# Kernel tuning notes

Hardware: AMD Instinct MI355X
Metric: run time of the kernel (lower is better)

Reference implementation:

```python
import jax, jax.numpy as jnp
import numpy as np

ALPHA = 0.2  # LeakyReLU negative slope
NEG_INF = -9e15


def setup_inputs() -> dict:
    key = jax.random.key(0)
    ks = jax.random.split(key, 6)
    B, N, F_in, F_out = 16, 1024, 1024, 512
    x = jax.random.normal(ks[0], (B, N, F_in), dtype=jnp.float32)
    adj = jax.random.randint(ks[1], (B, N, N), 0, 2, dtype=jnp.int32)
    W = jax.random.normal(ks[2], (F_in, F_out), dtype=jnp.float32) * 0.02
    a = jax.random.normal(ks[3], (2 * F_out, 1), dtype=jnp.float32) * 0.02
    fc_w = jax.random.normal(ks[4], (F_out, 2 * F_out), dtype=jnp.float32) * 0.02
    fc_b = jnp.zeros((F_out,), dtype=jnp.float32)
    return {"x": x, "adj": adj, "W": W, "a": a, "fc_w": fc_w, "fc_b": fc_b}


def reference(x, adj, W, a, fc_w, fc_b):
    # h: [B, N, F_out]
    h = jnp.matmul(x, W)
    F_out = W.shape[1]
    # The original builds a_input = concat(h_i, h_j) of shape [B,N,N,2F] and
    # contracts with a. Equivalently (same math, no O(N^2 F) intermediate):
    # e_ij = leakyrelu(h_i . a[:F] + h_j . a[F:])
    a1 = a[:F_out, 0]  # [F_out]
    a2 = a[F_out:, 0]  # [F_out]
    f1 = jnp.einsum('bnf,f->bn', h, a1)  # source term
    f2 = jnp.einsum('bnf,f->bn', h, a2)  # target term
    e = jax.nn.leaky_relu(f1[:, :, None] + f2[:, None, :], negative_slope=ALPHA)  # [B,N,N]
    attention = jnp.where(adj > 0, e, jnp.full_like(e, NEG_INF))
    attention = jax.nn.softmax(attention, axis=2)
    # dropout is identity in eval mode
    agg = jnp.matmul(attention, h)  # [B,N,F_out]
    h_prime = jnp.concatenate([agg, h], axis=2)  # [B,N,2F]
    h_prime = jnp.matmul(h_prime, fc_w.T) + fc_b
    return jax.nn.elu(h_prime)  # concat=True path
```

## Files before the change

kernel.cpp:

```cpp
#include <hip/hip_runtime.h>

#define ALPHA 0.2f

typedef __attribute__((ext_vector_type(8))) short short8;
typedef __attribute__((ext_vector_type(4))) float f32x4;

__device__ __forceinline__ unsigned short f2b(float f) {
  unsigned int u; __builtin_memcpy(&u, &f, 4);
  unsigned int r = (u + 0x7FFFu + ((u >> 16) & 1u)) >> 16;
  return (unsigned short)r;
}
__device__ __forceinline__ float b2f(unsigned short v) {
  unsigned int u = ((unsigned int)v) << 16; float f; __builtin_memcpy(&f, &u, 4); return f;
}
__device__ __forceinline__ void gl_lds16(const unsigned short* g, unsigned short* l) {
  __builtin_amdgcn_global_load_lds((__attribute__((address_space(1))) void*)g,
                                   (__attribute__((address_space(3))) void*)l, 16, 0, 0);
}
__device__ __forceinline__ void vm6() { asm volatile("s_waitcnt vmcnt(6)" ::: "memory"); }
__device__ __forceinline__ void vm0() { asm volatile("s_waitcnt vmcnt(0)" ::: "memory"); }
__device__ __forceinline__ void lg0() { asm volatile("s_waitcnt lgkmcnt(0)" ::: "memory"); }

__device__ __forceinline__ void cvt_f4(const float* __restrict__ in,
                                       unsigned short* __restrict__ out,
                                       unsigned int f4idx) {
  float4 v = ((const float4*)in)[f4idx];
  alignas(8) unsigned short o[4];
  o[0] = f2b(v.x); o[1] = f2b(v.y); o[2] = f2b(v.z); o[3] = f2b(v.w);
  ((uint2*)out)[f4idx] = *(const uint2*)o;
}

__global__ __launch_bounds__(256) void prep1(const float* __restrict__ x,
                                             unsigned short* __restrict__ xb,
                                             const float* __restrict__ fcw,
                                             unsigned short* __restrict__ fcwb,
                                             const float* __restrict__ W,
                                             unsigned short* __restrict__ Wt) {
  __shared__ alignas(16) unsigned short tile[64][72];
  unsigned int bx = blockIdx.x;
  unsigned int tid = threadIdx.x;
  if (bx < 8192u) {
    unsigned int base = bx * 512u;
    cvt_f4(x, xb, base + tid);
    cvt_f4(x, xb, base + 256u + tid);
  } else if (bx < 8448u) {
    unsigned int base = (bx - 8192u) * 512u;
    cvt_f4(fcw, fcwb, base + tid);
    cvt_f4(fcw, fcwb, base + 256u + tid);
  } else {
    unsigned int idx = bx - 8448u;
    unsigned int k0 = (idx >> 3) * 64, n0 = (idx & 7) * 64;
    #pragma unroll
    for (int p = 0; p < 4; p++) {
      int r = p * 16 + (tid >> 4);
      int c = (tid & 15) * 4;
      float4 v = *(const float4*)(W + (size_t)(k0 + r) * 512 + n0 + c);
      tile[r][c] = f2b(v.x); tile[r][c + 1] = f2b(v.y);
      tile[r][c + 2] = f2b(v.z); tile[r][c + 3] = f2b(v.w);
    }
    __syncthreads();
    int f = tid >> 2;
    int ic = (tid & 3) * 16;
    alignas(16) unsigned short buf[16];
    #pragma unroll
    for (int k = 0; k < 16; k++) buf[k] = tile[ic + k][f];
    uint4* dst = (uint4*)(Wt + (size_t)(n0 + f) * 1024 + k0 + ic);
    dst[0] = ((const uint4*)buf)[0];
    dst[1] = ((const uint4*)buf)[1];
  }
}

__global__ __launch_bounds__(256) void prep2(const unsigned short* __restrict__ hp,
                                             const float* __restrict__ a,
                                             float* __restrict__ f1, float* __restrict__ f2,
                                             unsigned short* __restrict__ ht) {
  __shared__ alignas(16) unsigned short tile[64][72];
  int bx = blockIdx.x;
  int tid = threadIdx.x;
  if (bx < 4096) {
    int row = bx * 4 + (tid >> 6);
    int lane = tid & 63;
    const unsigned short* hrow = hp + (size_t)row * 1024 + 512;
    uint4 raw = *(const uint4*)(hrow + lane * 8);
    alignas(16) unsigned short hv[8]; __builtin_memcpy(hv, &raw, 16);
    float s1 = 0.f, s2 = 0.f;
    #pragma unroll
    for (int j = 0; j < 8; j++) {
      float hf = b2f(hv[j]);
      s1 += hf * a[lane * 8 + j];
      s2 += hf * a[512 + lane * 8 + j];
    }
    #pragma unroll
    for (int o = 32; o > 0; o >>= 1) { s1 += __shfl_down(s1, o); s2 += __shfl_down(s2, o); }
    if (lane == 0) { f1[row] = s1; f2[row] = s2; }
  } else {
    int idx = bx - 4096;
    int b = idx >> 7;
    int f0 = ((idx >> 4) & 7) * 64;
    int i0 = (idx & 15) * 64;
    #pragma unroll
    for (int p = 0; p < 2; p++) {
      int r = p * 32 + (tid >> 3);
      int c = (tid & 7) * 8;
      uint4 v = *(const uint4*)(hp + (size_t)(b * 1024 + i0 + r) * 1024 + 512 + f0 + c);
      *(uint4*)(&tile[r][c]) = v;
    }
    __syncthreads();
    int f = tid >> 2;
    int ic = (tid & 3) * 16;
    alignas(16) unsigned short buf[16];
    #pragma unroll
    for (int k = 0; k < 16; k++) buf[k] = tile[ic + k][f];
    uint4* dst = (uint4*)(ht + (size_t)(b * 512 + f0 + f) * 1024 + i0 + ic);
    dst[0] = ((const uint4*)buf)[0];
    dst[1] = ((const uint4*)buf)[1];
  }
}

__global__ __launch_bounds__(256) void rowsum_P(const int* __restrict__ adj,
                                                const float* __restrict__ f1,
                                                const float* __restrict__ f2,
                                                float* __restrict__ invl,
                                                unsigned short* __restrict__ P) {
  int row = blockIdx.x * 4 + (threadIdx.x >> 6);
  int lane = threadIdx.x & 63;
  int b = row >> 10;
  float f1v = f1[row];
  const int4* ap = (const int4*)(adj + (size_t)row * 1024) + lane * 4;
  int4 a0 = ap[0];
  int4 a1 = ap[1];
  int4 a2 = ap[2];
  int4 a3 = ap[3];
  int av[16] = {a0.x, a0.y, a0.z, a0.w, a1.x, a1.y, a1.z, a1.w,
                a2.x, a2.y, a2.z, a2.w, a3.x, a3.y, a3.z, a3.w};
  const float* f2p = f2 + (b << 10) + lane * 16;
  float4 v0 = ((const float4*)f2p)[0];
  float4 v1 = ((const float4*)f2p)[1];
  float4 v2 = ((const float4*)f2p)[2];
  float4 v3 = ((const float4*)f2p)[3];
  float fv[16] = {v0.x, v0.y, v0.z, v0.w, v1.x, v1.y, v1.z, v1.w,
                  v2.x, v2.y, v2.z, v2.w, v3.x, v3.y, v3.z, v3.w};
  float s = 0.f;
  alignas(16) unsigned short o[16];
  #pragma unroll
  for (int j = 0; j < 16; j++) {
    float p = 0.f;
    if (av[j] > 0) {
      float z = f1v + fv[j];
      z = z > 0.f ? z : ALPHA * z;
      p = __expf(z);
      s += p;
    }
    o[j] = f2b(p);
  }
  uint4* dst = (uint4*)(P + (size_t)row * 1024 + lane * 16);
  dst[0] = ((const uint4*)o)[0];
  dst[1] = ((const uint4*)o)[1];
  #pragma unroll
  for (int off = 32; off > 0; off >>= 1) s += __shfl_down(s, off);
  if (lane == 0) invl[row] = 1.0f / s;
}

template <int EPI>
__global__ __launch_bounds__(512, 2) void gemm_bt(
    const unsigned short* __restrict__ A, size_t aBS,
    const unsigned short* __restrict__ Bt, size_t bBS,
    int K,
    void* __restrict__ outp, size_t oBS, int ldo, int ocol,
    const float* __restrict__ scale,
    const float* __restrict__ bias) {
  __shared__ alignas(16) unsigned short As[2 * 128 * 64];
  __shared__ alignas(16) unsigned short Bs[2 * 256 * 64];
  const int tid = threadIdx.x;
  const int lane = tid & 63;
  const int w = tid >> 6;
  const int m0 = blockIdx.x * 128;
  const int n0 = blockIdx.y * 256;
  const int zb = blockIdx.z;
  const unsigned short* Ab = A + (size_t)zb * aBS;
  const unsigned short* Btb = Bt + (size_t)zb * bBS;

  f32x4 acc[4][4];
  #pragma unroll
  for (int i = 0; i < 4; i++)
    #pragma unroll
    for (int j = 0; j < 4; j++)
      #pragma unroll
      for (int r = 0; r < 4; r++) acc[i][j][r] = 0.f;

  const int lr = lane >> 3;
  const int lc = (lane & 7) ^ lr;
  const unsigned short* ag = Ab + (size_t)(m0 + w * 8 + lr) * K + lc * 8;
  const unsigned short* bg = Btb + (size_t)(n0 + w * 8 + lr) * K + lc * 8;
  const int asb = w * 8 * 64;
  const int bsb = w * 8 * 64;

  const int wm = (w & 1) * 64;
  const int wn = (w >> 1) * 64;
  const int row16 = lane & 15;
  const int quad = lane >> 4;
  const int sw = row16 & 7;

  const int nk = K >> 6;

  #pragma unroll
  for (int t = 0; t < 2; t++)
    gl_lds16(ag + (size_t)(t * 64) * K, As + t * 4096 + asb);
  #pragma unroll
  for (int t = 0; t < 4; t++)
    gl_lds16(bg + (size_t)(t * 64) * K, Bs + t * 4096 + bsb);
  #pragma unroll
  for (int t = 0; t < 2; t++)
    gl_lds16(ag + 64 + (size_t)(t * 64) * K, As + 8192 + t * 4096 + asb);
  #pragma unroll
  for (int t = 0; t < 4; t++)
    gl_lds16(bg + 64 + (size_t)(t * 64) * K, Bs + 16384 + t * 4096 + bsb);
  vm6();
  __builtin_amdgcn_s_barrier();

  for (int k = 0; k < nk; k++) {
    const int ab = (k & 1) * 8192;
    const int bb = (k & 1) * 16384;
    const bool st2 = (k + 2 < nk);
    const bool pub = (k + 1 < nk);

    short8 af[2][4], bf[2][4];
    #pragma unroll
    for (int s = 0; s < 2; s++) {
      #pragma unroll
      for (int i = 0; i < 4; i++) {
        af[s][i] = *(const short8*)(As + ab + (wm + i * 16 + row16) * 64 + ((s * 4 + quad) ^ sw) * 8);
        bf[s][i] = *(const short8*)(Bs + bb + (wn + i * 16 + row16) * 64 + ((s * 4 + quad) ^ sw) * 8);
      }
    }
    lg0();
    __builtin_amdgcn_s_barrier();

    if (st2) {
      const int ko = (k + 2) * 64;
      #pragma unroll
      for (int t = 0; t < 2; t++)
        gl_lds16(ag + ko + (size_t)(t * 64) * K, As + ab + t * 4096 + asb);
      #pragma unroll
      for (int t = 0; t < 4; t++)
        gl_lds16(bg + ko + (size_t)(t * 64) * K, Bs + bb + t * 4096 + bsb);
    }

    __builtin_amdgcn_s_setprio(1);
    #pragma unroll
    for (int s = 0; s < 2; s++)
      #pragma unroll
      for (int am = 0; am < 4; am++)
        #pragma unroll
        for (int bn = 0; bn < 4; bn++)
          acc[am][bn] = __builtin_amdgcn_mfma_f32_16x16x32_bf16(af[s][am], bf[s][bn], acc[am][bn], 0, 0, 0);
    __builtin_amdgcn_s_setprio(0);

    if (pub) {
      if (st2) vm6(); else vm0();
      __builtin_amdgcn_s_barrier();
    }
  }

  const int col = lane & 15;
  const int r0 = quad * 4;
  #pragma unroll
  for (int am = 0; am < 4; am++) {
    #pragma unroll
    for (int bn = 0; bn < 4; bn++) {
      #pragma unroll
      for (int r = 0; r < 4; r++) {
        int m = m0 + wm + am * 16 + r0 + r;
        int n = n0 + wn + bn * 16 + col;
        float v = acc[am][bn][r];
        if (EPI == 3) v *= scale[zb * 1024 + m];
        if (EPI == 2) {
          v += bias[n];
          v = v > 0.f ? v : expm1f(v);
          ((float*)outp)[(size_t)m * ldo + n] = v;
        } else {
          ((unsigned short*)outp)[(size_t)zb * oBS + (size_t)m * ldo + ocol + n] = f2b(v);
        }
      }
    }
  }
}

extern "C" void kernel_launch(void* const* d_in, const int* in_sizes, int n_in,
                              void* d_out, int out_size, void* d_ws, size_t ws_size,
                              hipStream_t stream) {
  const float* x   = (const float*)d_in[0];
  const int*   adj = (const int*)d_in[1];
  const float* W   = (const float*)d_in[2];
  const float* a   = (const float*)d_in[3];
  const float* fcw = (const float*)d_in[4];
  const float* fcb = (const float*)d_in[5];
  float* out = (float*)d_out;
  char* ws = (char*)d_ws;

  unsigned short* xb   = (unsigned short*)(ws);
  unsigned short* hp   = (unsigned short*)(ws + 33554432);
  unsigned short* ht   = (unsigned short*)(ws + 67108864);
  unsigned short* Wt   = (unsigned short*)(ws + 83886080);
  unsigned short* fcwb = (unsigned short*)(ws + 84934656);
  float* f1            = (float*)(ws + 85983232);
  float* f2            = (float*)(ws + 86048768);
  float* invl          = (float*)(ws + 86114304);
  unsigned short* P = xb;

  prep1<<<8576, 256, 0, stream>>>(x, xb, fcw, fcwb, W, Wt);

  gemm_bt<1><<<dim3(128, 2, 1), 512, 0, stream>>>(xb, 0, Wt, 0, 1024,
                                                  hp, 0, 1024, 512, nullptr, nullptr);
  prep2<<<6144, 256, 0, stream>>>(hp, a, f1, f2, ht);
  rowsum_P<<<4096, 256, 0, stream>>>(adj, f1, f2, invl, P);

  gemm_bt<3><<<dim3(8, 2, 16), 512, 0, stream>>>(P, 1024 * 1024, ht, 512 * 1024, 1024,
                                                 hp, 1024 * 1024, 1024, 0, invl, nullptr);
  gemm_bt<2><<<dim3(128, 2, 1), 512, 0, stream>>>(hp, 0, fcwb, 0, 1024,
                                                  out, 0, 512, 0, nullptr, fcb);
}
```

Measured before the change: 259.0 us.

## Fuse x bf16 conversion into first GEMM and emit transposed h from epilogue

The first GEMM now reads fp32 x directly and converts it to bf16 in registers before writing to LDS, which removes the separate conversion pass over x and its bf16 round trip through memory. The same GEMM's epilogue writes a transposed bf16 copy of h through shared memory, so prep2 no longer needs its transpose blocks. This lowers memory traffic and launch work. In exchange the A-operand loads in the main loop become register loads plus explicit LDS stores, with extra waitcnt handling that could reduce pipelining efficiency.

```diff
diff --git a/kernel.cpp b/kernel.cpp
--- a/kernel.cpp
+++ b/kernel.cpp
@@ -17,7 +17,15 @@
   __builtin_amdgcn_global_load_lds((__attribute__((address_space(1))) void*)g,
                                    (__attribute__((address_space(3))) void*)l, 16, 0, 0);
 }
+__device__ __forceinline__ uint4 pack8(float4 v0, float4 v1) {
+  alignas(16) unsigned short o[8];
+  o[0] = f2b(v0.x); o[1] = f2b(v0.y); o[2] = f2b(v0.z); o[3] = f2b(v0.w);
+  o[4] = f2b(v1.x); o[5] = f2b(v1.y); o[6] = f2b(v1.z); o[7] = f2b(v1.w);
+  return *(const uint4*)o;
+}
+__device__ __forceinline__ void vm8() { asm volatile("s_waitcnt vmcnt(8)" ::: "memory"); }
 __device__ __forceinline__ void vm6() { asm volatile("s_waitcnt vmcnt(6)" ::: "memory"); }
+__device__ __forceinline__ void vm4() { asm volatile("s_waitcnt vmcnt(4)" ::: "memory"); }
 __device__ __forceinline__ void vm0() { asm volatile("s_waitcnt vmcnt(0)" ::: "memory"); }
 __device__ __forceinline__ void lg0() { asm volatile("s_waitcnt lgkmcnt(0)" ::: "memory"); }
 
@@ -30,25 +38,19 @@
   ((uint2*)out)[f4idx] = *(const uint2*)o;
 }
 
-__global__ __launch_bounds__(256) void prep1(const float* __restrict__ x,
-                                             unsigned short* __restrict__ xb,
-                                             const float* __restrict__ fcw,
+__global__ __launch_bounds__(256) void prep1(const float* __restrict__ fcw,
                                              unsigned short* __restrict__ fcwb,
                                              const float* __restrict__ W,
                                              unsigned short* __restrict__ Wt) {
   __shared__ alignas(16) unsigned short tile[64][72];
   unsigned int bx = blockIdx.x;
   unsigned int tid = threadIdx.x;
-  if (bx < 8192u) {
+  if (bx < 256u) {
     unsigned int base = bx * 512u;
-    cvt_f4(x, xb, base + tid);
-    cvt_f4(x, xb, base + 256u + tid);
-  } else if (bx < 8448u) {
-    unsigned int base = (bx - 8192u) * 512u;
     cvt_f4(fcw, fcwb, base + tid);
     cvt_f4(fcw, fcwb, base + 256u + tid);
   } else {
-    unsigned int idx = bx - 8448u;
+    unsigned int idx = bx - 256u;
     unsigned int k0 = (idx >> 3) * 64, n0 = (idx & 7) * 64;
     #pragma unroll
     for (int p = 0; p < 4; p++) {
@@ -72,49 +74,22 @@
 
 __global__ __launch_bounds__(256) void prep2(const unsigned short* __restrict__ hp,
                                              const float* __restrict__ a,
-                                             float* __restrict__ f1, float* __restrict__ f2,
-                                             unsigned short* __restrict__ ht) {
-  __shared__ alignas(16) unsigned short tile[64][72];
-  int bx = blockIdx.x;
-  int tid = threadIdx.x;
-  if (bx < 4096) {
-    int row = bx * 4 + (tid >> 6);
-    int lane = tid & 63;
-    const unsigned short* hrow = hp + (size_t)row * 1024 + 512;
-    uint4 raw = *(const uint4*)(hrow + lane * 8);
-    alignas(16) unsigned short hv[8]; __builtin_memcpy(hv, &raw, 16);
-    float s1 = 0.f, s2 = 0.f;
-    #pragma unroll
-    for (int j = 0; j < 8; j++) {
-      float hf = b2f(hv[j]);
-      s1 += hf * a[lane * 8 + j];
-      s2 += hf * a[512 + lane * 8 + j];
-    }
-    #pragma unroll
-    for (int o = 32; o > 0; o >>= 1) { s1 += __shfl_down(s1, o); s2 += __shfl_down(s2, o); }
-    if (lane == 0) { f1[row] = s1; f2[row] = s2; }
-  } else {
-    int idx = bx - 4096;
-    int b = idx >> 7;
-    int f0 = ((idx >> 4) & 7) * 64;
-    int i0 = (idx & 15) * 64;
-    #pragma unroll
-    for (int p = 0; p < 2; p++) {
-      int r = p * 32 + (tid >> 3);
-      int c = (tid & 7) * 8;
-      uint4 v = *(const uint4*)(hp + (size_t)(b * 1024 + i0 + r) * 1024 + 512 + f0 + c);
-      *(uint4*)(&tile[r][c]) = v;
-    }
-    __syncthreads();
-    int f = tid >> 2;
-    int ic = (tid & 3) * 16;
-    alignas(16) unsigned short buf[16];
-    #pragma unroll
-    for (int k = 0; k < 16; k++) buf[k] = tile[ic + k][f];
-    uint4* dst = (uint4*)(ht + (size_t)(b * 512 + f0 + f) * 1024 + i0 + ic);
-    dst[0] = ((const uint4*)buf)[0];
-    dst[1] = ((const uint4*)buf)[1];
-  }
+                                             float* __restrict__ f1, float* __restrict__ f2) {
+  int row = blockIdx.x * 4 + (threadIdx.x >> 6);
+  int lane = threadIdx.x & 63;
+  const unsigned short* hrow = hp + (size_t)row * 1024 + 512;
+  uint4 raw = *(const uint4*)(hrow + lane * 8);
+  alignas(16) unsigned short hv[8]; __builtin_memcpy(hv, &raw, 16);
+  float s1 = 0.f, s2 = 0.f;
+  #pragma unroll
+  for (int j = 0; j < 8; j++) {
+    float hf = b2f(hv[j]);
+    s1 += hf * a[lane * 8 + j];
+    s2 += hf * a[512 + lane * 8 + j];
+  }
+  #pragma unroll
+  for (int o = 32; o > 0; o >>= 1) { s1 += __shfl_down(s1, o); s2 += __shfl_down(s2, o); }
+  if (lane == 0) { f1[row] = s1; f2[row] = s2; }
 }
 
 __global__ __launch_bounds__(256) void rowsum_P(const int* __restrict__ adj,
@@ -161,23 +136,24 @@
   if (lane == 0) invl[row] = 1.0f / s;
 }
 
-template <int EPI>
+template <int EPI, int CVTA>
 __global__ __launch_bounds__(512, 2) void gemm_bt(
-    const unsigned short* __restrict__ A, size_t aBS,
+    const void* __restrict__ A_, size_t aBS,
     const unsigned short* __restrict__ Bt, size_t bBS,
     int K,
     void* __restrict__ outp, size_t oBS, int ldo, int ocol,
     const float* __restrict__ scale,
-    const float* __restrict__ bias) {
-  __shared__ alignas(16) unsigned short As[2 * 128 * 64];
-  __shared__ alignas(16) unsigned short Bs[2 * 256 * 64];
+    const float* __restrict__ bias,
+    unsigned short* __restrict__ htout) {
+  __shared__ alignas(16) unsigned short smem[49152];
+  unsigned short* As = smem;
+  unsigned short* Bs = smem + 16384;
   const int tid = threadIdx.x;
   const int lane = tid & 63;
   const int w = tid >> 6;
   const int m0 = blockIdx.x * 128;
   const int n0 = blockIdx.y * 256;
   const int zb = blockIdx.z;
-  const unsigned short* Ab = A + (size_t)zb * aBS;
   const unsigned short* Btb = Bt + (size_t)zb * bBS;
 
   f32x4 acc[4][4];
@@ -190,10 +166,16 @@
 
   const int lr = lane >> 3;
   const int lc = (lane & 7) ^ lr;
-  const unsigned short* ag = Ab + (size_t)(m0 + w * 8 + lr) * K + lc * 8;
+  const unsigned short* ag = nullptr;
+  const float* agf = nullptr;
+  if (CVTA)
+    agf = (const float*)A_ + (size_t)(m0 + w * 8 + lr) * K + lc * 8;
+  else
+    ag = (const unsigned short*)A_ + (size_t)zb * aBS + (size_t)(m0 + w * 8 + lr) * K + lc * 8;
   const unsigned short* bg = Btb + (size_t)(n0 + w * 8 + lr) * K + lc * 8;
-  const int asb = w * 8 * 64;
-  const int bsb = w * 8 * 64;
+  const int asb = w * 512;
+  const int bsb = w * 512;
+  const int aw = asb + lane * 8;
 
   const int wm = (w & 1) * 64;
   const int wn = (w >> 1) * 64;
@@ -203,19 +185,48 @@
 
   const int nk = K >> 6;
 
-  #pragma unroll
-  for (int t = 0; t < 2; t++)
-    gl_lds16(ag + (size_t)(t * 64) * K, As + t * 4096 + asb);
-  #pragma unroll
-  for (int t = 0; t < 4; t++)
-    gl_lds16(bg + (size_t)(t * 64) * K, Bs + t * 4096 + bsb);
-  #pragma unroll
-  for (int t = 0; t < 2; t++)
-    gl_lds16(ag + 64 + (size_t)(t * 64) * K, As + 8192 + t * 4096 + asb);
-  #pragma unroll
-  for (int t = 0; t < 4; t++)
-    gl_lds16(bg + 64 + (size_t)(t * 64) * K, Bs + 16384 + t * 4096 + bsb);
-  vm6();
+  if (CVTA) {
+    float4 a0[2][2], a1[2][2];
+    #pragma unroll
+    for (int t = 0; t < 2; t++) {
+      a0[t][0] = *(const float4*)(agf + (size_t)(t * 64) * K);
+      a0[t][1] = *(const float4*)(agf + (size_t)(t * 64) * K + 4);
+    }
+    #pragma unroll
+    for (int t = 0; t < 4; t++)
+      gl_lds16(bg + (size_t)(t * 64) * K, Bs + t * 4096 + bsb);
+    #pragma unroll
+    for (int t = 0; t < 2; t++) {
+      a1[t][0] = *(const float4*)(agf + 64 + (size_t)(t * 64) * K);
+      a1[t][1] = *(const float4*)(agf + 64 + (size_t)(t * 64) * K + 4);
+    }
+    #pragma unroll
+    for (int t = 0; t < 4; t++)
+      gl_lds16(bg + 64 + (size_t)(t * 64) * K, Bs + 16384 + t * 4096 + bsb);
+    vm8();
+    #pragma unroll
+    for (int t = 0; t < 2; t++)
+      *(uint4*)(As + t * 4096 + aw) = pack8(a0[t][0], a0[t][1]);
+    vm4();
+    #pragma unroll
+    for (int t = 0; t < 2; t++)
+      *(uint4*)(As + 8192 + t * 4096 + aw) = pack8(a1[t][0], a1[t][1]);
+  } else {
+    #pragma unroll
+    for (int t = 0; t < 2; t++)
+      gl_lds16(ag + (size_t)(t * 64) * K, As + t * 4096 + asb);
+    #pragma unroll
+    for (int t = 0; t < 4; t++)
+      gl_lds16(bg + (size_t)(t * 64) * K, Bs + t * 4096 + bsb);
+    #pragma unroll
+    for (int t = 0; t < 2; t++)
+      gl_lds16(ag + 64 + (size_t)(t * 64) * K, As + 8192 + t * 4096 + asb);
+    #pragma unroll
+    for (int t = 0; t < 4; t++)
+      gl_lds16(bg + 64 + (size_t)(t * 64) * K, Bs + 16384 + t * 4096 + bsb);
+    vm6();
+  }
+  lg0();
   __builtin_amdgcn_s_barrier();
 
   for (int k = 0; k < nk; k++) {
@@ -236,11 +247,20 @@
     lg0();
     __builtin_amdgcn_s_barrier();
 
+    float4 av[2][2];
     if (st2) {
       const int ko = (k + 2) * 64;
-      #pragma unroll
-      for (int t = 0; t < 2; t++)
-        gl_lds16(ag + ko + (size_t)(t * 64) * K, As + ab + t * 4096 + asb);
+      if (CVTA) {
+        #pragma unroll
+        for (int t = 0; t < 2; t++) {
+          av[t][0] = *(const float4*)(agf + ko + (size_t)(t * 64) * K);
+          av[t][1] = *(const float4*)(agf + ko + (size_t)(t * 64) * K + 4);
+        }
+      } else {
+        #pragma unroll
+        for (int t = 0; t < 2; t++)
+          gl_lds16(ag + ko + (size_t)(t * 64) * K, As + ab + t * 4096 + asb);
+      }
       #pragma unroll
       for (int t = 0; t < 4; t++)
         gl_lds16(bg + ko + (size_t)(t * 64) * K, Bs + bb + t * 4096 + bsb);
@@ -257,7 +277,19 @@
     __builtin_amdgcn_s_setprio(0);
 
     if (pub) {
-      if (st2) vm6(); else vm0();
+      if (CVTA) {
+        if (st2) {
+          vm4();
+          #pragma unroll
+          for (int t = 0; t < 2; t++)
+            *(uint4*)(As + ab + t * 4096 + aw) = pack8(av[t][0], av[t][1]);
+        } else {
+          vm0();
+        }
+        lg0();
+      } else {
+        if (st2) vm6(); else vm0();
+      }
       __builtin_amdgcn_s_barrier();
     }
   }
@@ -284,6 +316,31 @@
       }
     }
   }
+
+  if (EPI == 1) {
+    __syncthreads();
+    #pragma unroll
+    for (int am = 0; am < 4; am++)
+      #pragma unroll
+      for (int bn = 0; bn < 4; bn++)
+        #pragma unroll
+        for (int r = 0; r < 4; r++) {
+          int mloc = wm + am * 16 + r0 + r;
+          int nloc = wn + bn * 16 + col;
+          smem[nloc * 136 + mloc] = f2b(acc[am][bn][r]);
+        }
+    __syncthreads();
+    const int b = m0 >> 10;
+    const int i0 = m0 & 1023;
+    unsigned short* htp = htout + ((size_t)(b * 512 + n0) << 10) + i0;
+    #pragma unroll
+    for (int p = 0; p < 8; p++) {
+      int f = p * 32 + (tid >> 4);
+      int ib = (tid & 15) * 8;
+      uint4 v = *(const uint4*)(smem + f * 136 + ib);
+      *(uint4*)(htp + ((size_t)f << 10) + ib) = v;
+    }
+  }
 }
 
 extern "C" void kernel_launch(void* const* d_in, const int* in_sizes, int n_in,
@@ -298,7 +355,7 @@
   float* out = (float*)d_out;
   char* ws = (char*)d_ws;
 
-  unsigned short* xb   = (unsigned short*)(ws);
+  unsigned short* P    = (unsigned short*)(ws);
   unsigned short* hp   = (unsigned short*)(ws + 33554432);
   unsigned short* ht   = (unsigned short*)(ws + 67108864);
   unsigned short* Wt   = (unsigned short*)(ws + 83886080);
@@ -306,17 +363,16 @@
   float* f1            = (float*)(ws + 85983232);
   float* f2            = (float*)(ws + 86048768);
   float* invl          = (float*)(ws + 86114304);
-  unsigned short* P = xb;
-
-  prep1<<<8576, 256, 0, stream>>>(x, xb, fcw, fcwb, W, Wt);
-
-  gemm_bt<1><<<dim3(128, 2, 1), 512, 0, stream>>>(xb, 0, Wt, 0, 1024,
-                                                  hp, 0, 1024, 512, nullptr, nullptr);
-  prep2<<<6144, 256, 0, stream>>>(hp, a, f1, f2, ht);
+
+  prep1<<<384, 256, 0, stream>>>(fcw, fcwb, W, Wt);
+
+  gemm_bt<1, 1><<<dim3(128, 2, 1), 512, 0, stream>>>(x, 0, Wt, 0, 1024,
+                                                     hp, 0, 1024, 512, nullptr, nullptr, ht);
+  prep2<<<4096, 256, 0, stream>>>(hp, a, f1, f2);
   rowsum_P<<<4096, 256, 0, stream>>>(adj, f1, f2, invl, P);
 
-  gemm_bt<3><<<dim3(8, 2, 16), 512, 0, stream>>>(P, 1024 * 1024, ht, 512 * 1024, 1024,
-                                                 hp, 1024 * 1024, 1024, 0, invl, nullptr);
-  gemm_bt<2><<<dim3(128, 2, 1), 512, 0, stream>>>(hp, 0, fcwb, 0, 1024,
-                                                  out, 0, 512, 0, nullptr, fcb);
-}
+  gemm_bt<3, 0><<<dim3(8, 2, 16), 512, 0, stream>>>(P, 1024 * 1024, ht, 512 * 1024, 1024,
+                                                    hp, 1024 * 1024, 1024, 0, invl, nullptr, nullptr);
+  gemm_bt<2, 0><<<dim3(128, 2, 1), 512, 0, stream>>>(hp, 0, fcwb, 0, 1024,
+                                                     out, 0, 512, 0, nullptr, fcb, nullptr);
+}
```

Result: no change. 259.5 us (+0.2%).
